# Kernel tuning notes

Hardware: AMD Instinct MI355X
Metric: run time of the kernel (lower is better)

## Reference

```python
import jax, jax.numpy as jnp
import numpy as np

MAX_DISP = 4  # displacement radius -> 9x9 = 81 shifts


def setup_inputs() -> dict:
    key = jax.random.key(0)
    k1, k2 = jax.random.split(key)
    B, C, H, W = 8, 256, 96, 160
    tensorFirst = jax.random.normal(k1, (B, C, H, W), dtype=jnp.float32)
    tensorSecond = jax.random.normal(k2, (B, C, H, W), dtype=jnp.float32)
    return {"tensorFirst": tensorFirst, "tensorSecond": tensorSecond}


def reference(tensorFirst, tensorSecond):
    # Multi-displacement cross-correlation cost volume (FlowNet/PWC-Net style).
    # For each of the 81 displacements (dy, dx) in [-4, 4]^2:
    #   out[b, i*9+j, y, x] = mean_c( input1[b,c,y,x] * input2[b,c,y+dy,x+dx] )
    # (zero-padded outside the image), matching the torch fallback exactly
    # (sum over channels / channels == mean over channels).
    B, C, H, W = tensorFirst.shape
    p2 = jnp.pad(
        tensorSecond,
        ((0, 0), (0, 0), (MAX_DISP, MAX_DISP), (MAX_DISP, MAX_DISP)),
    )
    outs = []
    for dy in range(-MAX_DISP, MAX_DISP + 1):  # fixed 9-step loop (static shifts)
        for dx in range(-MAX_DISP, MAX_DISP + 1):
            shifted = p2[:, :, MAX_DISP + dy:MAX_DISP + dy + H,
                         MAX_DISP + dx:MAX_DISP + dx + W]
            outs.append(jnp.mean(tensorFirst * shifted, axis=1))  # [B, H, W]
    return jnp.stack(outs, axis=1)  # [B, 81, H, W]
```

## Files before the change

kernel.cpp:

```cpp
#include <hip/hip_runtime.h>
#include <hip/hip_fp16.h>

#define CH 256
#define HH 96
#define WW 160
#define HW (HH * WW)

typedef _Float16 half8 __attribute__((ext_vector_type(8)));
typedef float f32x4 __attribute__((ext_vector_type(4)));

__device__ inline unsigned pk2f(float a, float b) {
    return (unsigned)__half_as_ushort(__float2half(a)) |
           ((unsigned)__half_as_ushort(__float2half(b)) << 16);
}

__global__ __launch_bounds__(256, 4)
void corr_v3(const float* __restrict__ Fp, const float* __restrict__ Sp,
             float* __restrict__ out) {
    __shared__ uint4 sS[12 * 128];

    const int bid = blockIdx.x;
    const int b   = bid & 7;
    const int rem = bid >> 3;
    const int y0  = (rem / 10) * 4;
    const int x0  = (rem % 10) * 16;

    const int t    = threadIdx.x;
    const int lane = t & 63;
    const int wv   = t >> 6;
    const int q    = lane >> 4;
    const int n    = lane & 15;

    const float* Fb = Fp + (size_t)b * CH * HW;
    const float* Sb = Sp + (size_t)b * CH * HW;

    const int np = lane & 7;
    const int qq = (lane >> 3) & 3;
    const int jt = (lane >> 5) & 1;
    const int gx = x0 - 4 + jt * 16 + np * 2;
    const bool xok = (gx >= 0) & (gx + 1 < WW);

    f32x4 acc[9][2];
#pragma unroll
    for (int dy = 0; dy < 9; dy++) {
        f32x4 z = {0.f, 0.f, 0.f, 0.f};
        acc[dy][0] = z;
        acc[dy][1] = z;
    }

    for (int ch = 0; ch < 8; ch++) {
        const int c0 = ch * 32;

        const float* fp0 = Fb + (size_t)(c0 + q * 8) * HW + (y0 + wv) * WW + x0 + n;
        float fa[8];
#pragma unroll
        for (int j = 0; j < 8; j++) fa[j] = fp0[(size_t)j * HW];

        uint4 pk[3][2];
#pragma unroll
        for (int i = 0; i < 3; i++) {
            const int row = i * 4 + wv;
            const int gy  = y0 - 4 + row;
            const bool ok = ((unsigned)gy < HH) & xok;
            const size_t off = ok ? ((size_t)(c0 + qq * 8) * HW +
                                     (size_t)gy * WW + gx) : 0;
            const float2* p2 = (const float2*)(Sb + off);
            float2 ld[8];
#pragma unroll
            for (int j = 0; j < 8; j++) {
                float2 v = p2[(size_t)j * (HW / 2)];
                ld[j].x = ok ? v.x : 0.0f;
                ld[j].y = ok ? v.y : 0.0f;
            }
            pk[i][0].x = pk2f(ld[0].x, ld[1].x);
            pk[i][0].y = pk2f(ld[2].x, ld[3].x);
            pk[i][0].z = pk2f(ld[4].x, ld[5].x);
            pk[i][0].w = pk2f(ld[6].x, ld[7].x);
            pk[i][1].x = pk2f(ld[0].y, ld[1].y);
            pk[i][1].y = pk2f(ld[2].y, ld[3].y);
            pk[i][1].z = pk2f(ld[4].y, ld[5].y);
            pk[i][1].w = pk2f(ld[6].y, ld[7].y);
        }

        half8 av;
#pragma unroll
        for (int j = 0; j < 8; j++) av[j] = (_Float16)fa[j];

        __syncthreads();
#pragma unroll
        for (int i = 0; i < 3; i++) {
            uint4* dst = &sS[(i * 4 + wv) * 128 + lane * 2];
            dst[0] = pk[i][0];
            dst[1] = pk[i][1];
        }
        __syncthreads();

#pragma unroll
        for (int dy = 0; dy < 9; dy++) {
            const int row = wv + dy;
            half8 b0 = *(const half8*)(sS + row * 128 + lane);
            half8 b1 = *(const half8*)(sS + row * 128 + 64 + lane);
            acc[dy][0] = __builtin_amdgcn_mfma_f32_16x16x32_f16(av, b0, acc[dy][0], 0, 0, 0);
            acc[dy][1] = __builtin_amdgcn_mfma_f32_16x16x32_f16(av, b1, acc[dy][1], 0, 0, 0);
        }
    }

    const int y = y0 + wv;
#pragma unroll
    for (int r = 0; r < 4; r++) {
        const int m = q * 4 + r;
#pragma unroll
        for (int jtt = 0; jtt < 2; jtt++) {
            const int dxp = jtt * 16 + n - m;
            if (dxp >= 0 && dxp <= 8) {
                float* p = out + ((size_t)(b * 81 + dxp) * HH + y) * WW + x0 + m;
#pragma unroll
                for (int dy = 0; dy < 9; dy++) {
                    p[(size_t)dy * 9 * HW] = acc[dy][jtt][r] * (1.0f / 256.0f);
                }
            }
        }
    }
}

extern "C" void kernel_launch(void* const* d_in, const int* in_sizes, int n_in,
                              void* d_out, int out_size, void* d_ws, size_t ws_size,
                              hipStream_t stream) {
    const float* F = (const float*)d_in[0];
    const float* S = (const float*)d_in[1];
    float* o = (float*)d_out;
    corr_v3<<<dim3(1920), dim3(256), 0, stream>>>(F, S, o);
}
```

Before: 330.7 us.

## Prefetch next channel chunk into registers while MFMAs run

Global loads for the next 32-channel chunk of both inputs are issued into raw registers right after the shared-memory stores, so their latency overlaps with the current chunk's MFMA loop. Pointer and bounds computations are hoisted out of the channel loop and advanced incrementally. The extra live registers lead to relaxing the launch-bounds occupancy hint from 4 to 3 blocks per CU, which reduces latency hiding across waves and may add a scheduling tail.

```diff
diff --git a/kernel.cpp b/kernel.cpp
--- a/kernel.cpp
+++ b/kernel.cpp
@@ -14,8 +14,8 @@
            ((unsigned)__half_as_ushort(__float2half(b)) << 16);
 }
 
-__global__ __launch_bounds__(256, 4)
-void corr_v3(const float* __restrict__ Fp, const float* __restrict__ Sp,
+__global__ __launch_bounds__(256, 3)
+void corr_v4(const float* __restrict__ Fp, const float* __restrict__ Sp,
              float* __restrict__ out) {
     __shared__ uint4 sS[12 * 128];
 
@@ -40,6 +40,36 @@
     const int gx = x0 - 4 + jt * 16 + np * 2;
     const bool xok = (gx >= 0) & (gx + 1 < WW);
 
+    bool okv[3];
+    const float2* pS[3];
+#pragma unroll
+    for (int i = 0; i < 3; i++) {
+        const int row = i * 4 + wv;
+        const int gy  = y0 - 4 + row;
+        okv[i] = ((unsigned)gy < HH) & xok;
+        const size_t off = okv[i] ? ((size_t)(qq * 8) * HW +
+                                     (size_t)gy * WW + gx) : 0;
+        pS[i] = (const float2*)(Sb + off);
+    }
+    const float* pF = Fb + (size_t)(q * 8) * HW + (y0 + wv) * WW + x0 + n;
+
+    float2 rawS[3][8];
+    float  rawF[8];
+
+    auto load_raw = [&]() {
+#pragma unroll
+        for (int i = 0; i < 3; i++)
+#pragma unroll
+            for (int j = 0; j < 8; j++)
+                rawS[i][j] = pS[i][(size_t)j * (HW / 2)];
+#pragma unroll
+        for (int j = 0; j < 8; j++)
+            rawF[j] = pF[(size_t)j * HW];
+#pragma unroll
+        for (int i = 0; i < 3; i++) pS[i] += (size_t)16 * HW;
+        pF += (size_t)32 * HW;
+    };
+
     f32x4 acc[9][2];
 #pragma unroll
     for (int dy = 0; dy < 9; dy++) {
@@ -48,52 +78,39 @@
         acc[dy][1] = z;
     }
 
+    load_raw();
+
+#pragma unroll 1
     for (int ch = 0; ch < 8; ch++) {
-        const int c0 = ch * 32;
+        __syncthreads();
 
-        const float* fp0 = Fb + (size_t)(c0 + q * 8) * HW + (y0 + wv) * WW + x0 + n;
-        float fa[8];
+        half8 av;
 #pragma unroll
-        for (int j = 0; j < 8; j++) fa[j] = fp0[(size_t)j * HW];
-
-        uint4 pk[3][2];
+        for (int j = 0; j < 8; j++) av[j] = (_Float16)rawF[j];
 #pragma unroll
         for (int i = 0; i < 3; i++) {
-            const int row = i * 4 + wv;
-            const int gy  = y0 - 4 + row;
-            const bool ok = ((unsigned)gy < HH) & xok;
-            const size_t off = ok ? ((size_t)(c0 + qq * 8) * HW +
-                                     (size_t)gy * WW + gx) : 0;
-            const float2* p2 = (const float2*)(Sb + off);
             float2 ld[8];
 #pragma unroll
             for (int j = 0; j < 8; j++) {
-                float2 v = p2[(size_t)j * (HW / 2)];
-                ld[j].x = ok ? v.x : 0.0f;
-                ld[j].y = ok ? v.y : 0.0f;
+                ld[j].x = okv[i] ? rawS[i][j].x : 0.0f;
+                ld[j].y = okv[i] ? rawS[i][j].y : 0.0f;
             }
-            pk[i][0].x = pk2f(ld[0].x, ld[1].x);
-            pk[i][0].y = pk2f(ld[2].x, ld[3].x);
-            pk[i][0].z = pk2f(ld[4].x, ld[5].x);
-            pk[i][0].w = pk2f(ld[6].x, ld[7].x);
-            pk[i][1].x = pk2f(ld[0].y, ld[1].y);
-            pk[i][1].y = pk2f(ld[2].y, ld[3].y);
-            pk[i][1].z = pk2f(ld[4].y, ld[5].y);
-            pk[i][1].w = pk2f(ld[6].y, ld[7].y);
-        }
-
-        half8 av;
-#pragma unroll
-        for (int j = 0; j < 8; j++) av[j] = (_Float16)fa[j];
-
-        __syncthreads();
-#pragma unroll
-        for (int i = 0; i < 3; i++) {
+            uint4 v0, v1;
+            v0.x = pk2f(ld[0].x, ld[1].x);
+            v0.y = pk2f(ld[2].x, ld[3].x);
+            v0.z = pk2f(ld[4].x, ld[5].x);
+            v0.w = pk2f(ld[6].x, ld[7].x);
+            v1.x = pk2f(ld[0].y, ld[1].y);
+            v1.y = pk2f(ld[2].y, ld[3].y);
+            v1.z = pk2f(ld[4].y, ld[5].y);
+            v1.w = pk2f(ld[6].y, ld[7].y);
             uint4* dst = &sS[(i * 4 + wv) * 128 + lane * 2];
-            dst[0] = pk[i][0];
-            dst[1] = pk[i][1];
+            dst[0] = v0;
+            dst[1] = v1;
         }
         __syncthreads();
+
+        if (ch < 7) load_raw();
 
 #pragma unroll
         for (int dy = 0; dy < 9; dy++) {
@@ -129,5 +146,5 @@
     const float* F = (const float*)d_in[0];
     const float* S = (const float*)d_in[1];
     float* o = (float*)d_out;
-    corr_v3<<<dim3(1920), dim3(256), 0, stream>>>(F, S, o);
+    corr_v4<<<dim3(1920), dim3(256), 0, stream>>>(F, S, o);
 }
```

New measurement: 324.9 us. Within noise of the previous version (-1.7%).
